# Kernel optimization log

Measured on AMD Instinct MI355X. Metric: run time of the kernel, lower is better.

The kernel has to match this reference:

```python
import jax, jax.numpy as jnp
import numpy as np

BS, M, N = 256, 128, 1024
ITERS = 100
ALPHA = 0.1


def setup_inputs() -> dict:
    key = jax.random.key(0)
    k1, k2, k3, k4 = jax.random.split(key, 4)
    A = jax.random.normal(k1, (BS, M, N), dtype=jnp.float32)
    b = jax.random.normal(k2, (BS, M), dtype=jnp.float32)
    D1 = jax.random.normal(k3, (BS, N), dtype=jnp.float32)
    D2 = jax.random.normal(k4, (BS, N), dtype=jnp.float32)
    return {"A": A, "b": b, "D1": D1, "D2": D2, "bs": BS}


def _soft_thresholding(x, alpha, D1, D2):
    t = alpha * jnp.abs(D1)
    denom = 1.0 + 2.0 * alpha * D2 ** 2
    return jnp.where(x - t > 0, (x - t) / denom,
                     jnp.where(x + t < 0, (x + t) / denom, jnp.zeros_like(x)))


def reference(A, b, D1, D2, bs):
    n = D1.shape[1]
    # A is loop-invariant, so AAT^{-1} is identical every iteration; hoist it.
    AAT = jnp.einsum('bmn,bkn->bmk', A, A)          # (bs, m, m)
    AAT_inv = jnp.linalg.inv(AAT)

    def projection(y):
        Ay_minus_b = jnp.einsum('bmn,bn->bm', A, y) - b
        u = jnp.einsum('bmk,bk->bm', AAT_inv, Ay_minus_b)
        correction = jnp.einsum('bmn,bm->bn', A, u)  # A^T u
        return y - correction

    def step(carry, _):
        x, z = carry
        x_half = _soft_thresholding(z, ALPHA, D1, D2)
        x_new = projection(2.0 * x_half - z)
        z_new = z + x_new - x_half
        return (x_new, z_new), None

    x0 = jnp.zeros((bs, n), dtype=jnp.float32)
    z0 = jnp.zeros((bs, n), dtype=jnp.float32)
    (x, _), _ = jax.lax.scan(step, (x0, z0), None, length=ITERS)
    return x
```

## Files before the change

### kernel.cpp

```cpp
#include <hip/hip_runtime.h>
#include <math.h>

#define BS 256
#define MM 128
#define NN 1024
#define ITERS 100
#define ALPHA 0.1f
#define AST 129
#define IST 129
#define TRP 132

typedef _Float16 half8 __attribute__((ext_vector_type(8)));
typedef _Float16 half4 __attribute__((ext_vector_type(4)));
typedef _Float16 half2v __attribute__((ext_vector_type(2)));
typedef float f32x4 __attribute__((ext_vector_type(4)));

template <int CTRL>
__device__ __forceinline__ float dpp_add(float x) {
  int xi = __builtin_bit_cast(int, x);
  int r = __builtin_amdgcn_update_dpp(xi, xi, CTRL, 0xf, 0xf, true);
  return x + __builtin_bit_cast(float, r);
}

__global__ __attribute__((amdgpu_waves_per_eu(4, 4)))
__launch_bounds__(1024) void k_prep(const float* __restrict__ A,
                                    _Float16* __restrict__ ATh,
                                    _Float16* __restrict__ Gh) {
  __shared__ float As[64 * AST];
  __shared__ __align__(16) _Float16 Thi[8][2][64][8];
  __shared__ __align__(16) _Float16 Tlo[8][2][64][8];
  __shared__ float Msh[MM * IST];
  __shared__ float fcol[2][MM];
  __shared__ float frow[2][MM];

  int b = blockIdx.x;
  int tid = threadIdx.x;
  const float* Ab = A + (size_t)b * MM * NN;
  _Float16* ATb = ATh + (size_t)b * NN * MM;
  _Float16* Ghb = Gh + (size_t)b * MM * MM;

  {
    int lane = tid & 63;
    int w16 = tid >> 6;
    int wr = w16 & 3;
    int wc = w16 >> 2;
    int m0 = tid >> 4;
    int m1 = m0 + 64;
    int q0 = tid & 15;
    int kl = q0 * 4;
    int strip0 = m0 >> 4, strip1 = m1 >> 4;
    int kc_s = kl >> 5;
    int ln0 = (m0 & 15) + (((kl & 31) >> 3) << 4);
    int ln1 = (m1 & 15) + (((kl & 31) >> 3) << 4);
    int j0s = kl & 7;

    f32x4 acc[2][2];
#pragma unroll
    for (int i = 0; i < 2; ++i)
#pragma unroll
      for (int jj = 0; jj < 2; ++jj) acc[i][jj] = (f32x4){0.f, 0.f, 0.f, 0.f};

    auto stage = [&](int m, int strip, int ln, float4 v) {
      As[(kl + 0) * AST + m] = v.x;
      As[(kl + 1) * AST + m] = v.y;
      As[(kl + 2) * AST + m] = v.z;
      As[(kl + 3) * AST + m] = v.w;
      _Float16 h0 = (_Float16)v.x, h1 = (_Float16)v.y;
      _Float16 h2 = (_Float16)v.z, h3 = (_Float16)v.w;
      half4 hv = {h0, h1, h2, h3};
      half4 lv = {(_Float16)(v.x - (float)h0), (_Float16)(v.y - (float)h1),
                  (_Float16)(v.z - (float)h2), (_Float16)(v.w - (float)h3)};
      *(half4*)&Thi[strip][kc_s][ln][j0s] = hv;
      *(half4*)&Tlo[strip][kc_s][ln][j0s] = lv;
    };

    float4 va = *(const float4*)&Ab[(size_t)m0 * NN + kl];
    float4 vb = *(const float4*)&Ab[(size_t)m1 * NN + kl];

    for (int t = 0; t < 16; ++t) {
      int k0 = t * 64;
      stage(m0, strip0, ln0, va);
      stage(m1, strip1, ln1, vb);
      __syncthreads();
      if (t < 15) {
        int k0n = k0 + 64;
        va = *(const float4*)&Ab[(size_t)m0 * NN + k0n + kl];
        vb = *(const float4*)&Ab[(size_t)m1 * NN + k0n + kl];
      }
#pragma unroll
      for (int s = 0; s < 4; ++s) {
        int idx = tid + 1024 * s;
        int nl = idx >> 6;
        int mp = idx & 63;
        half2v hv;
        hv[0] = (_Float16)As[nl * AST + 2 * mp];
        hv[1] = (_Float16)As[nl * AST + 2 * mp + 1];
        *(half2v*)&ATb[(size_t)(k0 + nl) * MM + 2 * mp] = hv;
      }
#pragma unroll
      for (int kc = 0; kc < 2; ++kc) {
        half8 ahi[2], alo[2], bhi[2], blo[2];
#pragma unroll
        for (int i = 0; i < 2; ++i) {
          ahi[i] = *(const half8*)&Thi[2 * wr + i][kc][lane][0];
          alo[i] = *(const half8*)&Tlo[2 * wr + i][kc][lane][0];
          bhi[i] = *(const half8*)&Thi[2 * wc + i][kc][lane][0];
          blo[i] = *(const half8*)&Tlo[2 * wc + i][kc][lane][0];
        }
#pragma unroll
        for (int i = 0; i < 2; ++i)
#pragma unroll
          for (int jj = 0; jj < 2; ++jj) {
            acc[i][jj] = __builtin_amdgcn_mfma_f32_16x16x32_f16(
                ahi[i], bhi[jj], acc[i][jj], 0, 0, 0);
            acc[i][jj] = __builtin_amdgcn_mfma_f32_16x16x32_f16(
                ahi[i], blo[jj], acc[i][jj], 0, 0, 0);
            acc[i][jj] = __builtin_amdgcn_mfma_f32_16x16x32_f16(
                alo[i], bhi[jj], acc[i][jj], 0, 0, 0);
          }
      }
      __syncthreads();
    }
    int rbase = 4 * (lane >> 4), cbase = lane & 15;
#pragma unroll
    for (int i = 0; i < 2; ++i)
#pragma unroll
      for (int jj = 0; jj < 2; ++jj) {
        int r0 = (2 * wr + i) * 16 + rbase;
        int c0 = (2 * wc + jj) * 16 + cbase;
#pragma unroll
        for (int r_ = 0; r_ < 4; ++r_)
          Msh[(r0 + r_) * IST + c0] = acc[i][jj][r_];
      }
  }
  __syncthreads();

  {
    int j = tid & 127;
    int i0 = (tid >> 7) * 16;
    float m[16];
#pragma unroll
    for (int ii = 0; ii < 16; ++ii) m[ii] = Msh[(i0 + ii) * IST + j];
    if (tid < MM) {
      fcol[0][tid] = Msh[tid * IST];
      frow[0][tid] = Msh[tid];
    }
    __syncthreads();
    int cur = 0;
    for (int kb = 0; kb < 8; ++kb) {
#pragma unroll
      for (int kq = 0; kq < 16; ++kq) {
        int k = kb * 16 + kq;
        float p = 1.0f / fcol[cur][k];
        float mkj = frow[cur][j];
        float fik[16];
#pragma unroll
        for (int ii = 0; ii < 16; ++ii) fik[ii] = fcol[cur][i0 + ii];
        float pmkj = p * mkj;
        bool pivslab = (i0 == kb * 16);
        if (j == k) {
#pragma unroll
          for (int ii = 0; ii < 16; ++ii) m[ii] = -p * fik[ii];
          if (pivslab) m[kq] = p;
        } else {
#pragma unroll
          for (int ii = 0; ii < 16; ++ii) m[ii] = fmaf(-fik[ii], pmkj, m[ii]);
          if (pivslab) m[kq] = pmkj;
        }
        int nxt = cur ^ 1;
        if (k < MM - 1) {
          if (j == k + 1) {
#pragma unroll
            for (int ii = 0; ii < 16; ++ii) fcol[nxt][i0 + ii] = m[ii];
          }
          if (i0 == ((k + 1) & ~15)) frow[nxt][j] = m[(kq + 1) & 15];
        }
        __syncthreads();
        cur = nxt;
      }
    }
#pragma unroll
    for (int ii = 0; ii < 16; ++ii)
      Ghb[(size_t)(i0 + ii) * MM + j] = (_Float16)m[ii];
  }
}

__global__ __attribute__((amdgpu_waves_per_eu(4, 4)))
__launch_bounds__(1024) void k_main(
    const _Float16* __restrict__ AT, const _Float16* __restrict__ Gh,
    const float* __restrict__ bvec, const float* __restrict__ D1,
    const float* __restrict__ D2, float* __restrict__ out) {
  __shared__ __align__(16) _Float16 AL[512 * MM];
  __shared__ float2 tdi_sh[NN];
  __shared__ float b_sh[MM];
  __shared__ __align__(16) _Float16 s_h[MM];
  __shared__ __align__(16) _Float16 u_h[MM];
  __shared__ __align__(16) float t_redW[32][TRP];

  int b = blockIdx.x;
  int tid = threadIdx.x;
  const _Float16* ATb = AT + (size_t)b * NN * MM;
  const _Float16* Ghb = Gh + (size_t)b * MM * MM;

  int sub = tid & 7, rrow = tid >> 3;
  float ghf[8];
  {
    half8 g0 = *(const half8*)&Ghb[(size_t)rrow * MM + 16 * sub];
    half8 g1 = *(const half8*)&Ghb[(size_t)rrow * MM + 16 * sub + 8];
    f32x4 gA = __builtin_bit_cast(f32x4, g0);
    f32x4 gB = __builtin_bit_cast(f32x4, g1);
#pragma unroll
    for (int s = 0; s < 4; ++s) {
      ghf[s] = gA[s];
      ghf[4 + s] = gB[s];
    }
  }
#pragma unroll
  for (int s = 0; s < 8; ++s) asm volatile("" : "+v"(ghf[s]));
  {
    float d1 = D1[(size_t)b * NN + tid];
    float d2 = D2[(size_t)b * NN + tid];
    float2 td2;
    td2.x = ALPHA * fabsf(d1);
    td2.y = 1.0f / (1.0f + 2.0f * ALPHA * d2 * d2);
    tdi_sh[tid] = td2;
  }
  if (tid < MM) {
    float bb = bvec[(size_t)b * MM + tid];
    b_sh[tid] = bb;
    s_h[tid] = (_Float16)(-bb);
  }

  int l8 = tid & 7;
  int g = (tid >> 3) & 7;
  int w = tid >> 6;
  int mb = 16 * l8;
  int alsw = (g & 1) * 8;

#pragma unroll
  for (int i = 0; i < 8; ++i) {
    int c = tid + 1024 * i;
    int col = c >> 4;
    int m8 = (c & 15) * 8;
    int n = 32 * (col >> 5) + 32 + col;
    int phys = m8 ^ ((col & 1) << 3);
    *(half8*)&AL[col * MM + phys] = *(const half8*)&ATb[(size_t)n * MM + m8];
  }

  float rcw[16];
  {
    int n0 = 64 * w + 16 + g, n1 = 64 * w + 24 + g;
    f32x4 v0 = *(const f32x4*)&ATb[(size_t)n0 * MM + mb];
    f32x4 v1 = *(const f32x4*)&ATb[(size_t)n0 * MM + mb + 8];
    f32x4 v2 = *(const f32x4*)&ATb[(size_t)n1 * MM + mb];
    f32x4 v3 = *(const f32x4*)&ATb[(size_t)n1 * MM + mb + 8];
    rcw[0] = v0[0]; rcw[1] = v0[1]; rcw[2] = v0[2]; rcw[3] = v0[3];
    rcw[4] = v1[0]; rcw[5] = v1[1]; rcw[6] = v1[2]; rcw[7] = v1[3];
    rcw[8] = v2[0]; rcw[9] = v2[1]; rcw[10] = v2[2]; rcw[11] = v2[3];
    rcw[12] = v3[0]; rcw[13] = v3[1]; rcw[14] = v3[2]; rcw[15] = v3[3];
  }
#pragma unroll
  for (int k = 0; k < 16; ++k) asm volatile("" : "+v"(rcw[k]));

  float zz[8];
#pragma unroll
  for (int k = 0; k < 8; ++k) zz[k] = 0.0f;

  __syncthreads();

  for (int it = 0; it < ITERS; ++it) {
    bool last = (it == ITERS - 1);

    f32x4 sa0 = *(const f32x4*)&ATb[(size_t)(64 * w + g) * MM + mb];
    f32x4 sa1 = *(const f32x4*)&ATb[(size_t)(64 * w + g) * MM + mb + 8];
    f32x4 sb0 = *(const f32x4*)&ATb[(size_t)(64 * w + 8 + g) * MM + mb];
    f32x4 sb1 = *(const f32x4*)&ATb[(size_t)(64 * w + 8 + g) * MM + mb + 8];

    {
      int j0 = 16 * sub;
      half8 sA = *(const half8*)&s_h[j0];
      half8 sB = *(const half8*)&s_h[j0 + 8];
      float up = 0.0f;
      up = __builtin_amdgcn_fdot2(__builtin_bit_cast(half2v, ghf[0]),
                                  __builtin_shufflevector(sA, sA, 0, 1), up, false);
      up = __builtin_amdgcn_fdot2(__builtin_bit_cast(half2v, ghf[1]),
                                  __builtin_shufflevector(sA, sA, 2, 3), up, false);
      up = __builtin_amdgcn_fdot2(__builtin_bit_cast(half2v, ghf[2]),
                                  __builtin_shufflevector(sA, sA, 4, 5), up, false);
      up = __builtin_amdgcn_fdot2(__builtin_bit_cast(half2v, ghf[3]),
                                  __builtin_shufflevector(sA, sA, 6, 7), up, false);
      up = __builtin_amdgcn_fdot2(__builtin_bit_cast(half2v, ghf[4]),
                                  __builtin_shufflevector(sB, sB, 0, 1), up, false);
      up = __builtin_amdgcn_fdot2(__builtin_bit_cast(half2v, ghf[5]),
                                  __builtin_shufflevector(sB, sB, 2, 3), up, false);
      up = __builtin_amdgcn_fdot2(__builtin_bit_cast(half2v, ghf[6]),
                                  __builtin_shufflevector(sB, sB, 4, 5), up, false);
      up = __builtin_amdgcn_fdot2(__builtin_bit_cast(half2v, ghf[7]),
                                  __builtin_shufflevector(sB, sB, 6, 7), up, false);
      up = dpp_add<0xB1>(up);
      up = dpp_add<0x4E>(up);
      up = dpp_add<0x141>(up);
      if (sub == 0) u_h[rrow] = (_Float16)up;
    }
    __syncthreads();
    half8 uA = *(const half8*)&u_h[mb];
    half8 uB = *(const half8*)&u_h[mb + 8];
    half2v u0 = __builtin_shufflevector(uA, uA, 0, 1);
    half2v u1 = __builtin_shufflevector(uA, uA, 2, 3);
    half2v u2 = __builtin_shufflevector(uA, uA, 4, 5);
    half2v u3 = __builtin_shufflevector(uA, uA, 6, 7);
    half2v u4 = __builtin_shufflevector(uB, uB, 0, 1);
    half2v u5 = __builtin_shufflevector(uB, uB, 2, 3);
    half2v u6 = __builtin_shufflevector(uB, uB, 4, 5);
    half2v u7 = __builtin_shufflevector(uB, uB, 6, 7);

    float t[16];
#pragma unroll
    for (int k = 0; k < 16; ++k) t[k] = 0.0f;

    auto colstep = [&](half8 ha, half8 hb, int n, float zv) -> float {
      float cp = 0.0f;
      cp = __builtin_amdgcn_fdot2(__builtin_shufflevector(ha, ha, 0, 1), u0, cp, false);
      cp = __builtin_amdgcn_fdot2(__builtin_shufflevector(ha, ha, 2, 3), u1, cp, false);
      cp = __builtin_amdgcn_fdot2(__builtin_shufflevector(ha, ha, 4, 5), u2, cp, false);
      cp = __builtin_amdgcn_fdot2(__builtin_shufflevector(ha, ha, 6, 7), u3, cp, false);
      cp = __builtin_amdgcn_fdot2(__builtin_shufflevector(hb, hb, 0, 1), u4, cp, false);
      cp = __builtin_amdgcn_fdot2(__builtin_shufflevector(hb, hb, 2, 3), u5, cp, false);
      cp = __builtin_amdgcn_fdot2(__builtin_shufflevector(hb, hb, 4, 5), u6, cp, false);
      cp = __builtin_amdgcn_fdot2(__builtin_shufflevector(hb, hb, 6, 7), u7, cp, false);
      cp = dpp_add<0xB1>(cp);
      cp = dpp_add<0x4E>(cp);
      cp = dpp_add<0x141>(cp);
      float2 tdi = tdi_sh[n];
      float td = tdi.x, di = tdi.y;
      float xm = zv - td, xp = zv + td;
      float xh = xm > 0.0f ? xm * di : (xp < 0.0f ? xp * di : 0.0f);
      if (!last) {
        float z1 = xh - cp;
        float xm1 = z1 - td, xp1 = z1 + td;
        float xh1 = xm1 > 0.0f ? xm1 * di : (xp1 < 0.0f ? xp1 * di : 0.0f);
        float y = 2.0f * xh1 - z1;
        f32x4 wa = __builtin_bit_cast(f32x4, ha);
        f32x4 wb = __builtin_bit_cast(f32x4, hb);
#pragma unroll
        for (int i2 = 0; i2 < 4; ++i2) {
          asm("v_fma_mix_f32 %0, %1, %2, %0 op_sel_hi:[1,0,0]"
              : "+v"(t[2 * i2]) : "v"(wa[i2]), "v"(y));
          asm("v_fma_mix_f32 %0, %1, %2, %0 op_sel:[1,0,0] op_sel_hi:[1,0,0]"
              : "+v"(t[2 * i2 + 1]) : "v"(wa[i2]), "v"(y));
          asm("v_fma_mix_f32 %0, %1, %2, %0 op_sel_hi:[1,0,0]"
              : "+v"(t[8 + 2 * i2]) : "v"(wb[i2]), "v"(y));
          asm("v_fma_mix_f32 %0, %1, %2, %0 op_sel:[1,0,0] op_sel_hi:[1,0,0]"
              : "+v"(t[8 + 2 * i2 + 1]) : "v"(wb[i2]), "v"(y));
        }
        return z1;
      } else {
        float y = 2.0f * xh - zv;
        if (l8 == 0) out[(size_t)b * NN + n] = y - cp;
        return zv;
      }
    };

    {
      f32x4 ra = {rcw[0], rcw[1], rcw[2], rcw[3]};
      f32x4 rb = {rcw[4], rcw[5], rcw[6], rcw[7]};
      zz[0] = colstep(__builtin_bit_cast(half8, ra),
                      __builtin_bit_cast(half8, rb), 64 * w + 16 + g, zz[0]);
      f32x4 rc_ = {rcw[8], rcw[9], rcw[10], rcw[11]};
      f32x4 rd_ = {rcw[12], rcw[13], rcw[14], rcw[15]};
      zz[1] = colstep(__builtin_bit_cast(half8, rc_),
                      __builtin_bit_cast(half8, rd_), 64 * w + 24 + g, zz[1]);
    }
#pragma unroll
    for (int j = 0; j < 4; ++j) {
      const _Float16* ap = &AL[(32 * w + 8 * j + g) * MM];
      half8 ha = *(const half8*)&ap[mb + alsw];
      half8 hb = *(const half8*)&ap[mb + 8 - alsw];
      zz[2 + j] = colstep(ha, hb, 64 * w + 32 + 8 * j + g, zz[2 + j]);
    }
    zz[6] = colstep(__builtin_bit_cast(half8, sa0),
                    __builtin_bit_cast(half8, sa1), 64 * w + g, zz[6]);
    zz[7] = colstep(__builtin_bit_cast(half8, sb0),
                    __builtin_bit_cast(half8, sb1), 64 * w + 8 + g, zz[7]);

    if (!last) {
#pragma unroll
      for (int k = 0; k < 16; ++k) {
        t[k] = dpp_add<0x128>(t[k]);
        t[k] += __shfl_xor(t[k], 32);
      }
      if ((g & 5) == 0) {
        int row = 2 * w + (g >> 1);
#pragma unroll
        for (int s2 = 0; s2 < 4; ++s2) {
          f32x4 tv = {t[4 * s2], t[4 * s2 + 1], t[4 * s2 + 2], t[4 * s2 + 3]};
          *(f32x4*)&t_redW[row][mb + 4 * s2] = tv;
        }
      }
      __syncthreads();
      if (tid < MM) {
        float ssum = -b_sh[tid];
#pragma unroll
        for (int h = 0; h < 32; ++h) ssum += t_redW[h][tid];
        s_h[tid] = (_Float16)ssum;
      }
      __syncthreads();
    }
  }
}

extern "C" void kernel_launch(void* const* d_in, const int* in_sizes, int n_in,
                              void* d_out, int out_size, void* d_ws, size_t ws_size,
                              hipStream_t stream) {
  const float* A  = (const float*)d_in[0];
  const float* bv = (const float*)d_in[1];
  const float* D1 = (const float*)d_in[2];
  const float* D2 = (const float*)d_in[3];
  float* out = (float*)d_out;

  _Float16* ATh = (_Float16*)d_ws;
  _Float16* Gh = (_Float16*)((char*)d_ws + (size_t)BS * NN * MM * 2);

  k_prep<<<BS, 1024, 0, stream>>>(A, ATh, Gh);
  k_main<<<BS, 1024, 0, stream>>>(ATh, Gh, bv, D1, D2, out);
}
```

Baseline: 713.7 us.

## Split prep into separate Gram and inversion kernels, rewrite soft-threshold as clamp

The fused prep kernel becomes two kernels. k_aat uses 2 blocks of 512 threads per batch, each computing half the rows of A·A^T and half the transposed fp16 A; k_inv runs Gauss-Jordan inversion from the fp32 Gram matrix in global memory and writes fp16 in place. The aim is to let the Gram and inverse phases run at different occupancy and shorten the serialized prep per block, at the cost of an extra launch and a global round-trip of G. Soft-thresholding in the main loop is also rewritten as a branchless clamp, and the fcol reads are vectorised.

```diff
diff --git a/kernel.cpp b/kernel.cpp
--- a/kernel.cpp
+++ b/kernel.cpp
@@ -23,44 +23,47 @@
 }
 
 __global__ __attribute__((amdgpu_waves_per_eu(4, 4)))
-__launch_bounds__(1024) void k_prep(const float* __restrict__ A,
-                                    _Float16* __restrict__ ATh,
-                                    _Float16* __restrict__ Gh) {
+__launch_bounds__(512) void k_aat(const float* __restrict__ A,
+                                  float* __restrict__ G,
+                                  _Float16* __restrict__ ATh) {
   __shared__ float As[64 * AST];
   __shared__ __align__(16) _Float16 Thi[8][2][64][8];
   __shared__ __align__(16) _Float16 Tlo[8][2][64][8];
-  __shared__ float Msh[MM * IST];
-  __shared__ float fcol[2][MM];
-  __shared__ float frow[2][MM];
-
-  int b = blockIdx.x;
+  int b = blockIdx.x >> 1;
+  int p = blockIdx.x & 1;
   int tid = threadIdx.x;
   const float* Ab = A + (size_t)b * MM * NN;
+  float* Cb = G + (size_t)b * MM * MM;
   _Float16* ATb = ATh + (size_t)b * NN * MM;
-  _Float16* Ghb = Gh + (size_t)b * MM * MM;
-
-  {
-    int lane = tid & 63;
-    int w16 = tid >> 6;
-    int wr = w16 & 3;
-    int wc = w16 >> 2;
-    int m0 = tid >> 4;
-    int m1 = m0 + 64;
-    int q0 = tid & 15;
-    int kl = q0 * 4;
-    int strip0 = m0 >> 4, strip1 = m1 >> 4;
-    int kc_s = kl >> 5;
-    int ln0 = (m0 & 15) + (((kl & 31) >> 3) << 4);
-    int ln1 = (m1 & 15) + (((kl & 31) >> 3) << 4);
-    int j0s = kl & 7;
-
-    f32x4 acc[2][2];
-#pragma unroll
-    for (int i = 0; i < 2; ++i)
-#pragma unroll
-      for (int jj = 0; jj < 2; ++jj) acc[i][jj] = (f32x4){0.f, 0.f, 0.f, 0.f};
-
-    auto stage = [&](int m, int strip, int ln, float4 v) {
+
+  int lane = tid & 63;
+  int w = tid >> 6;
+  int wr = w & 1;
+  int wc = w >> 1;
+
+  f32x4 acc[2][2];
+#pragma unroll
+  for (int i = 0; i < 2; ++i)
+#pragma unroll
+    for (int jj = 0; jj < 2; ++jj) acc[i][jj] = (f32x4){0.f, 0.f, 0.f, 0.f};
+
+  float4 va[4];
+#pragma unroll
+  for (int s = 0; s < 4; ++s) {
+    int c = tid + s * 512;
+    int m = c >> 4;
+    int kl = (c & 15) * 4;
+    va[s] = *(const float4*)&Ab[(size_t)m * NN + kl];
+  }
+
+  for (int t = 0; t < 16; ++t) {
+    int k0 = t * 64;
+#pragma unroll
+    for (int s = 0; s < 4; ++s) {
+      int c = tid + s * 512;
+      int m = c >> 4;
+      int kl = (c & 15) * 4;
+      float4 v = va[s];
       As[(kl + 0) * AST + m] = v.x;
       As[(kl + 1) * AST + m] = v.y;
       As[(kl + 2) * AST + m] = v.z;
@@ -70,124 +73,145 @@
       half4 hv = {h0, h1, h2, h3};
       half4 lv = {(_Float16)(v.x - (float)h0), (_Float16)(v.y - (float)h1),
                   (_Float16)(v.z - (float)h2), (_Float16)(v.w - (float)h3)};
-      *(half4*)&Thi[strip][kc_s][ln][j0s] = hv;
-      *(half4*)&Tlo[strip][kc_s][ln][j0s] = lv;
-    };
-
-    float4 va = *(const float4*)&Ab[(size_t)m0 * NN + kl];
-    float4 vb = *(const float4*)&Ab[(size_t)m1 * NN + kl];
-
-    for (int t = 0; t < 16; ++t) {
-      int k0 = t * 64;
-      stage(m0, strip0, ln0, va);
-      stage(m1, strip1, ln1, vb);
+      int strip = m >> 4;
+      int kc = kl >> 5;
+      int ln = (m & 15) + (((kl & 31) >> 3) << 4);
+      int j0 = kl & 7;
+      *(half4*)&Thi[strip][kc][ln][j0] = hv;
+      *(half4*)&Tlo[strip][kc][ln][j0] = lv;
+    }
+    __syncthreads();
+    if (t < 15) {
+#pragma unroll
+      for (int s = 0; s < 4; ++s) {
+        int c = tid + s * 512;
+        int m = c >> 4;
+        int kl = (c & 15) * 4;
+        va[s] = *(const float4*)&Ab[(size_t)m * NN + k0 + 64 + kl];
+      }
+    }
+#pragma unroll
+    for (int s = 0; s < 4; ++s) {
+      int idx = tid + s * 512;
+      int nl = 32 * p + (idx >> 6);
+      int mp = idx & 63;
+      half2v hv;
+      hv[0] = (_Float16)As[nl * AST + 2 * mp];
+      hv[1] = (_Float16)As[nl * AST + 2 * mp + 1];
+      *(half2v*)&ATb[(size_t)(k0 + nl) * MM + 2 * mp] = hv;
+    }
+#pragma unroll
+    for (int kc = 0; kc < 2; ++kc) {
+      half8 ahi[2], alo[2], bhi[2], blo[2];
+#pragma unroll
+      for (int i = 0; i < 2; ++i) {
+        ahi[i] = *(const half8*)&Thi[4 * p + 2 * wr + i][kc][lane][0];
+        alo[i] = *(const half8*)&Tlo[4 * p + 2 * wr + i][kc][lane][0];
+        bhi[i] = *(const half8*)&Thi[2 * wc + i][kc][lane][0];
+        blo[i] = *(const half8*)&Tlo[2 * wc + i][kc][lane][0];
+      }
+#pragma unroll
+      for (int i = 0; i < 2; ++i)
+#pragma unroll
+        for (int jj = 0; jj < 2; ++jj) {
+          acc[i][jj] = __builtin_amdgcn_mfma_f32_16x16x32_f16(
+              ahi[i], bhi[jj], acc[i][jj], 0, 0, 0);
+          acc[i][jj] = __builtin_amdgcn_mfma_f32_16x16x32_f16(
+              ahi[i], blo[jj], acc[i][jj], 0, 0, 0);
+          acc[i][jj] = __builtin_amdgcn_mfma_f32_16x16x32_f16(
+              alo[i], bhi[jj], acc[i][jj], 0, 0, 0);
+        }
+    }
+    __syncthreads();
+  }
+  int rbase = 4 * (lane >> 4), cbase = lane & 15;
+#pragma unroll
+  for (int i = 0; i < 2; ++i)
+#pragma unroll
+    for (int jj = 0; jj < 2; ++jj) {
+      int r0 = (4 * p + 2 * wr + i) * 16 + rbase;
+      int c0 = (2 * wc + jj) * 16 + cbase;
+#pragma unroll
+      for (int r_ = 0; r_ < 4; ++r_)
+        Cb[(size_t)(r0 + r_) * MM + c0] = acc[i][jj][r_];
+    }
+}
+
+__global__ __attribute__((amdgpu_waves_per_eu(4, 4)))
+__launch_bounds__(1024) void k_inv(float* __restrict__ G) {
+  __shared__ float Msh[MM * IST];
+  __shared__ float fcol[2][MM];
+  __shared__ float frow[2][MM];
+  int b = blockIdx.x;
+  int tid = threadIdx.x;
+  float* Gb = G + (size_t)b * MM * MM;
+#pragma unroll
+  for (int s = 0; s < 4; ++s) {
+    int idx = (tid + s * 1024) * 4;
+    float4 v = *(const float4*)&Gb[idx];
+    int i = idx >> 7, j = idx & 127;
+    Msh[i * IST + j + 0] = v.x;
+    Msh[i * IST + j + 1] = v.y;
+    Msh[i * IST + j + 2] = v.z;
+    Msh[i * IST + j + 3] = v.w;
+  }
+  __syncthreads();
+  int j = tid & 127;
+  int i0 = (tid >> 7) * 16;
+  float m[16];
+#pragma unroll
+  for (int ii = 0; ii < 16; ++ii) m[ii] = Msh[(i0 + ii) * IST + j];
+  if (tid < MM) {
+    fcol[0][tid] = Msh[tid * IST];
+    frow[0][tid] = Msh[tid];
+  }
+  __syncthreads();
+  int cur = 0;
+  for (int kb = 0; kb < 8; ++kb) {
+#pragma unroll
+    for (int kq = 0; kq < 16; ++kq) {
+      int k = kb * 16 + kq;
+      float p = 1.0f / fcol[cur][k];
+      float mkj = frow[cur][j];
+      float fik[16];
+#pragma unroll
+      for (int q = 0; q < 4; ++q) {
+        f32x4 fv = *(const f32x4*)&fcol[cur][i0 + 4 * q];
+        fik[4 * q + 0] = fv[0]; fik[4 * q + 1] = fv[1];
+        fik[4 * q + 2] = fv[2]; fik[4 * q + 3] = fv[3];
+      }
+      float pmkj = p * mkj;
+      bool pivslab = (i0 == kb * 16);
+      if (j == k) {
+#pragma unroll
+        for (int ii = 0; ii < 16; ++ii) m[ii] = -p * fik[ii];
+        if (pivslab) m[kq] = p;
+      } else {
+#pragma unroll
+        for (int ii = 0; ii < 16; ++ii) m[ii] = fmaf(-fik[ii], pmkj, m[ii]);
+        if (pivslab) m[kq] = pmkj;
+      }
+      int nxt = cur ^ 1;
+      if (k < MM - 1) {
+        if (j == k + 1) {
+#pragma unroll
+          for (int ii = 0; ii < 16; ++ii) fcol[nxt][i0 + ii] = m[ii];
+        }
+        if (i0 == ((k + 1) & ~15)) frow[nxt][j] = m[(kq + 1) & 15];
+      }
       __syncthreads();
-      if (t < 15) {
-        int k0n = k0 + 64;
-        va = *(const float4*)&Ab[(size_t)m0 * NN + k0n + kl];
-        vb = *(const float4*)&Ab[(size_t)m1 * NN + k0n + kl];
-      }
-#pragma unroll
-      for (int s = 0; s < 4; ++s) {
-        int idx = tid + 1024 * s;
-        int nl = idx >> 6;
-        int mp = idx & 63;
-        half2v hv;
-        hv[0] = (_Float16)As[nl * AST + 2 * mp];
-        hv[1] = (_Float16)As[nl * AST + 2 * mp + 1];
-        *(half2v*)&ATb[(size_t)(k0 + nl) * MM + 2 * mp] = hv;
-      }
-#pragma unroll
-      for (int kc = 0; kc < 2; ++kc) {
-        half8 ahi[2], alo[2], bhi[2], blo[2];
-#pragma unroll
-        for (int i = 0; i < 2; ++i) {
-          ahi[i] = *(const half8*)&Thi[2 * wr + i][kc][lane][0];
-          alo[i] = *(const half8*)&Tlo[2 * wr + i][kc][lane][0];
-          bhi[i] = *(const half8*)&Thi[2 * wc + i][kc][lane][0];
-          blo[i] = *(const half8*)&Tlo[2 * wc + i][kc][lane][0];
-        }
-#pragma unroll
-        for (int i = 0; i < 2; ++i)
-#pragma unroll
-          for (int jj = 0; jj < 2; ++jj) {
-            acc[i][jj] = __builtin_amdgcn_mfma_f32_16x16x32_f16(
-                ahi[i], bhi[jj], acc[i][jj], 0, 0, 0);
-            acc[i][jj] = __builtin_amdgcn_mfma_f32_16x16x32_f16(
-                ahi[i], blo[jj], acc[i][jj], 0, 0, 0);
-            acc[i][jj] = __builtin_amdgcn_mfma_f32_16x16x32_f16(
-                alo[i], bhi[jj], acc[i][jj], 0, 0, 0);
-          }
-      }
-      __syncthreads();
-    }
-    int rbase = 4 * (lane >> 4), cbase = lane & 15;
-#pragma unroll
-    for (int i = 0; i < 2; ++i)
-#pragma unroll
-      for (int jj = 0; jj < 2; ++jj) {
-        int r0 = (2 * wr + i) * 16 + rbase;
-        int c0 = (2 * wc + jj) * 16 + cbase;
-#pragma unroll
-        for (int r_ = 0; r_ < 4; ++r_)
-          Msh[(r0 + r_) * IST + c0] = acc[i][jj][r_];
-      }
-  }
-  __syncthreads();
-
-  {
-    int j = tid & 127;
-    int i0 = (tid >> 7) * 16;
-    float m[16];
-#pragma unroll
-    for (int ii = 0; ii < 16; ++ii) m[ii] = Msh[(i0 + ii) * IST + j];
-    if (tid < MM) {
-      fcol[0][tid] = Msh[tid * IST];
-      frow[0][tid] = Msh[tid];
-    }
-    __syncthreads();
-    int cur = 0;
-    for (int kb = 0; kb < 8; ++kb) {
-#pragma unroll
-      for (int kq = 0; kq < 16; ++kq) {
-        int k = kb * 16 + kq;
-        float p = 1.0f / fcol[cur][k];
-        float mkj = frow[cur][j];
-        float fik[16];
-#pragma unroll
-        for (int ii = 0; ii < 16; ++ii) fik[ii] = fcol[cur][i0 + ii];
-        float pmkj = p * mkj;
-        bool pivslab = (i0 == kb * 16);
-        if (j == k) {
-#pragma unroll
-          for (int ii = 0; ii < 16; ++ii) m[ii] = -p * fik[ii];
-          if (pivslab) m[kq] = p;
-        } else {
-#pragma unroll
-          for (int ii = 0; ii < 16; ++ii) m[ii] = fmaf(-fik[ii], pmkj, m[ii]);
-          if (pivslab) m[kq] = pmkj;
-        }
-        int nxt = cur ^ 1;
-        if (k < MM - 1) {
-          if (j == k + 1) {
-#pragma unroll
-            for (int ii = 0; ii < 16; ++ii) fcol[nxt][i0 + ii] = m[ii];
-          }
-          if (i0 == ((k + 1) & ~15)) frow[nxt][j] = m[(kq + 1) & 15];
-        }
-        __syncthreads();
-        cur = nxt;
-      }
-    }
-#pragma unroll
-    for (int ii = 0; ii < 16; ++ii)
-      Ghb[(size_t)(i0 + ii) * MM + j] = (_Float16)m[ii];
-  }
+      cur = nxt;
+    }
+  }
+  _Float16* Ghb = (_Float16*)Gb;
+#pragma unroll
+  for (int ii = 0; ii < 16; ++ii)
+    Ghb[(size_t)(i0 + ii) * MM + j] = (_Float16)m[ii];
 }
 
 __global__ __attribute__((amdgpu_waves_per_eu(4, 4)))
 __launch_bounds__(1024) void k_main(
-    const _Float16* __restrict__ AT, const _Float16* __restrict__ Gh,
+    const _Float16* __restrict__ AT, const float* __restrict__ G,
     const float* __restrict__ bvec, const float* __restrict__ D1,
     const float* __restrict__ D2, float* __restrict__ out) {
   __shared__ __align__(16) _Float16 AL[512 * MM];
@@ -200,7 +224,7 @@
   int b = blockIdx.x;
   int tid = threadIdx.x;
   const _Float16* ATb = AT + (size_t)b * NN * MM;
-  const _Float16* Ghb = Gh + (size_t)b * MM * MM;
+  const _Float16* Ghb = (const _Float16*)(G + (size_t)b * MM * MM);
 
   int sub = tid & 7, rrow = tid >> 3;
   float ghf[8];
@@ -333,12 +357,12 @@
       cp = dpp_add<0x141>(cp);
       float2 tdi = tdi_sh[n];
       float td = tdi.x, di = tdi.y;
-      float xm = zv - td, xp = zv + td;
-      float xh = xm > 0.0f ? xm * di : (xp < 0.0f ? xp * di : 0.0f);
+      float xc = fminf(fmaxf(zv, -td), td);
+      float xh = (zv - xc) * di;
       if (!last) {
         float z1 = xh - cp;
-        float xm1 = z1 - td, xp1 = z1 + td;
-        float xh1 = xm1 > 0.0f ? xm1 * di : (xp1 < 0.0f ? xp1 * di : 0.0f);
+        float xc1 = fminf(fmaxf(z1, -td), td);
+        float xh1 = (z1 - xc1) * di;
         float y = 2.0f * xh1 - z1;
         f32x4 wa = __builtin_bit_cast(f32x4, ha);
         f32x4 wb = __builtin_bit_cast(f32x4, hb);
@@ -419,8 +443,9 @@
   float* out = (float*)d_out;
 
   _Float16* ATh = (_Float16*)d_ws;
-  _Float16* Gh = (_Float16*)((char*)d_ws + (size_t)BS * NN * MM * 2);
-
-  k_prep<<<BS, 1024, 0, stream>>>(A, ATh, Gh);
-  k_main<<<BS, 1024, 0, stream>>>(ATh, Gh, bv, D1, D2, out);
+  float* G = (float*)((char*)d_ws + (size_t)BS * NN * MM * 2);
+
+  k_aat<<<BS * 2, 512, 0, stream>>>(A, G, ATh);
+  k_inv<<<BS, 1024, 0, stream>>>(G);
+  k_main<<<BS, 1024, 0, stream>>>(ATh, G, bv, D1, D2, out);
 }
```

Measured after the change: 933.4 us. 1.31x slower.
